# Kernel optimization log

Measured on AMD Instinct MI355X. Metric: run time of the kernel, lower is better.

Reference implementation:

```python
import jax, jax.numpy as jnp
import numpy as np
import math

N_HEAD = 16

def setup_inputs() -> dict:
    key = jax.random.key(0)
    k1, k2, k3, k4, k5 = jax.random.split(key, 5)
    B, T, C = 8, 1024, 1024
    scale = 0.02
    return {
        "x": jax.random.normal(k1, (B, T, C), dtype=jnp.float32),
        "w_attn": jax.random.normal(k2, (C, 3 * C), dtype=jnp.float32) * scale,
        "b_attn": jax.random.normal(k3, (3 * C,), dtype=jnp.float32) * scale,
        "w_proj": jax.random.normal(k4, (C, C), dtype=jnp.float32) * scale,
        "b_proj": jax.random.normal(k5, (C,), dtype=jnp.float32) * scale,
    }

def reference(x, w_attn, b_attn, w_proj, b_proj):
    B, T, C = x.shape
    H = N_HEAD
    hd = C // H
    # QKV projection: [B,T,3C]
    qkv = jnp.einsum("btc,cd->btd", x, w_attn) + b_attn
    q, k, v = jnp.split(qkv, 3, axis=-1)
    # [B,T,C] -> [B,H,T,hd]
    def heads(t):
        return t.reshape(B, T, H, hd).transpose(0, 2, 1, 3)
    q, k, v = heads(q), heads(k), heads(v)
    # scaled QK^T: [B,H,T,T]
    att = jnp.einsum("bhqd,bhkd->bhqk", q, k) * (1.0 / math.sqrt(hd))
    # causal mask (tril of block_size cropped to T)
    causal = jnp.tril(jnp.ones((T, T), dtype=bool))
    att = jnp.where(causal, att, jnp.float32(-jnp.inf))
    att = jax.nn.softmax(att, axis=-1)
    # attention-weighted values: [B,H,T,hd] -> [B,T,C]
    y = jnp.einsum("bhqk,bhkd->bhqd", att, v)
    y = y.transpose(0, 2, 1, 3).reshape(B, T, C)
    # output projection
    return jnp.einsum("btc,cd->btd", y, w_proj) + b_proj
```

## Files before the change

### kernel.cpp

```cpp
#include <hip/hip_runtime.h>

typedef __bf16 bf16x8 __attribute__((ext_vector_type(8)));
typedef float f32x4 __attribute__((ext_vector_type(4)));
typedef unsigned short u16;
typedef unsigned int u32;
typedef unsigned long long u64;

__device__ __forceinline__ u16 f2bf(float f) {
  u32 u = __builtin_bit_cast(u32, f);
  u32 r = (u + 0x7FFFu + ((u >> 16) & 1u)) >> 16;
  return (u16)r;
}

__device__ __forceinline__ void gload_lds16(const u16* g, u16* l) {
  __builtin_amdgcn_global_load_lds(
      (const __attribute__((address_space(1))) u32*)g,
      (__attribute__((address_space(3))) u32*)l, 16, 0, 0);
}

__global__ void cast_x_kernel(const float* __restrict__ in, u16* __restrict__ out, int n4) {
  int i = blockIdx.x * blockDim.x + threadIdx.x;
  if (i >= n4) return;
  float4 v = ((const float4*)in)[i];
  uint2 o;
  o.x = (u32)f2bf(v.x) | ((u32)f2bf(v.y) << 16);
  o.y = (u32)f2bf(v.z) | ((u32)f2bf(v.w) << 16);
  ((uint2*)out)[i] = o;
}

__global__ void transpose_cast_kernel(const float* __restrict__ in, u16* __restrict__ out,
                                      int K, int N) {
  __shared__ float tile[32][33];
  int n0 = blockIdx.x * 32, k0 = blockIdx.y * 32;
  int tx = threadIdx.x & 31, ty = threadIdx.x >> 5;
#pragma unroll
  for (int i = 0; i < 32; i += 8)
    tile[ty + i][tx] = in[(size_t)(k0 + ty + i) * N + n0 + tx];
  __syncthreads();
#pragma unroll
  for (int i = 0; i < 32; i += 8)
    out[(size_t)(n0 + ty + i) * K + k0 + tx] = f2bf(tile[tx][ty + i]);
}

template <int MODE>
__global__ __launch_bounds__(256, 3) void gemm_bf16(
    const u16* __restrict__ A, const u16* __restrict__ Bt,
    const float* __restrict__ bias, u16* __restrict__ out_q,
    float* __restrict__ out_f, int M, int N, int K) {
  __shared__ alignas(16) u16 As[128 * 64];
  __shared__ alignas(16) u16 Bs[128 * 64];
  const int tiles_n = N >> 7;
  const int bid0 = blockIdx.x;
  const int cpx = (int)gridDim.x >> 3;
  const int swz = (bid0 & 7) * cpx + (bid0 >> 3);
  const int tm = swz / tiles_n;
  const int tn = swz % tiles_n;
  const int tid = threadIdx.x;
  const int wave = tid >> 6, lane = tid & 63;
  const int wr = (wave >> 1) * 64, wc = (wave & 1) * 64;
  const int lr = lane & 15, lg = lane >> 4;

  f32x4 acc[4][4] = {};
  const size_t a_base = (size_t)(tm * 128) * K;
  const size_t b_base = (size_t)(tn * 128) * K;

  for (int k0 = 0; k0 < K; k0 += 64) {
#pragma unroll
    for (int i = 0; i < 4; ++i) {
      int c = i * 256 + tid;
      int row = c >> 3, ch = c & 7;
      int sw = (ch ^ (row & 7)) * 8;
      gload_lds16(A + a_base + (size_t)row * K + k0 + sw, &As[c * 8]);
      gload_lds16(Bt + b_base + (size_t)row * K + k0 + sw, &Bs[c * 8]);
    }
    __syncthreads();
    bf16x8 af[4][2], bfr[4][2];
#pragma unroll
    for (int m = 0; m < 4; ++m) {
      int row = wr + m * 16 + lr;
#pragma unroll
      for (int kk = 0; kk < 2; ++kk)
        af[m][kk] = *(const bf16x8*)&As[(row * 64 + kk * 32 + lg * 8) ^ ((row & 7) << 3)];
    }
#pragma unroll
    for (int n = 0; n < 4; ++n) {
      int row = wc + n * 16 + lr;
#pragma unroll
      for (int kk = 0; kk < 2; ++kk)
        bfr[n][kk] = *(const bf16x8*)&Bs[(row * 64 + kk * 32 + lg * 8) ^ ((row & 7) << 3)];
    }
#pragma unroll
    for (int m = 0; m < 4; ++m)
#pragma unroll
      for (int n = 0; n < 4; ++n) {
        if constexpr (MODE == 0) {
          acc[m][n] = __builtin_amdgcn_mfma_f32_16x16x32_bf16(bfr[n][0], af[m][0], acc[m][n], 0, 0, 0);
          acc[m][n] = __builtin_amdgcn_mfma_f32_16x16x32_bf16(bfr[n][1], af[m][1], acc[m][n], 0, 0, 0);
        } else {
          acc[m][n] = __builtin_amdgcn_mfma_f32_16x16x32_bf16(af[m][0], bfr[n][0], acc[m][n], 0, 0, 0);
          acc[m][n] = __builtin_amdgcn_mfma_f32_16x16x32_bf16(af[m][1], bfr[n][1], acc[m][n], 0, 0, 0);
        }
      }
    __syncthreads();
  }

  if constexpr (MODE == 0) {
    const int tok0 = tm * 128 + wr;
    const int col0 = tn * 128 + wc;
#pragma unroll
    for (int n = 0; n < 4; ++n) {
      int ncol = col0 + n * 16 + lg * 4;
      float4 bv = *(const float4*)&bias[ncol];
      int which = ncol >> 10, c = ncol & 1023;
      int h = c >> 6, d = c & 63;
#pragma unroll
      for (int m = 0; m < 4; ++m) {
        int tok = tok0 + m * 16 + lr;
        int b = tok >> 10, t = tok & 1023;
        union { u16 s[4]; uint2 v; } pk;
        pk.s[0] = f2bf(acc[m][n][0] + bv.x);
        pk.s[1] = f2bf(acc[m][n][1] + bv.y);
        pk.s[2] = f2bf(acc[m][n][2] + bv.z);
        pk.s[3] = f2bf(acc[m][n][3] + bv.w);
        *(uint2*)&out_q[(size_t)which * 8388608 + ((((size_t)b * 16 + h) * 1024 + t) << 6) + d] = pk.v;
      }
    }
  } else if constexpr (MODE == 2) {
    const int tok0 = tm * 128 + wr;
    const int col0 = tn * 128 + wc;
#pragma unroll
    for (int n = 0; n < 4; ++n) {
      int ncol = col0 + n * 16 + lr;
      float bv = bias[ncol];
      int h = ncol >> 6, d = ncol & 63;
#pragma unroll
      for (int m = 0; m < 4; ++m) {
        int t0 = tok0 + m * 16 + lg * 4;
        int b = t0 >> 10, t = t0 & 1023;
        union { u16 s[4]; uint2 v; } pk;
        pk.s[0] = f2bf(acc[m][n][0] + bv);
        pk.s[1] = f2bf(acc[m][n][1] + bv);
        pk.s[2] = f2bf(acc[m][n][2] + bv);
        pk.s[3] = f2bf(acc[m][n][3] + bv);
        *(uint2*)&out_q[(((size_t)b * 16 + h) * 64 + d) * 1024 + t] = pk.v;
      }
    }
  } else {
    const int row0 = tm * 128 + wr;
    const int col0 = tn * 128 + wc;
#pragma unroll
    for (int n = 0; n < 4; ++n) {
      int col = col0 + n * 16 + lr;
      float bv = bias[col];
#pragma unroll
      for (int m = 0; m < 4; ++m)
#pragma unroll
        for (int r = 0; r < 4; ++r) {
          int mrow = row0 + m * 16 + lg * 4 + r;
          out_f[(size_t)mrow * N + col] = acc[m][n][r] + bv;
        }
    }
  }
}

__global__ __launch_bounds__(256, 2) void attn_kernel(
    const u16* __restrict__ Qb, const u16* __restrict__ Kb,
    const u16* __restrict__ Vb, u16* __restrict__ yb) {
  __shared__ alignas(16) u16 Ks[128 * 64];
  __shared__ alignas(16) u16 Vt[64 * 128];
  __shared__ alignas(16) u16 Pl[4][32 * 64];

  const int bid = blockIdx.x;
  const int xcd = bid & 7, j = bid >> 3;
  const int bh = ((j >> 2) << 3) + xcd;
  const int pr = j & 3;
  const size_t hb = (size_t)bh * 65536;
  const int tid = threadIdx.x, w = tid >> 6, lane = tid & 63;
  const int lr = lane & 15, lg = lane >> 4;
  const int b = bh >> 4, h = bh & 15;
  const float C2 = 0.18033688011112042f;

  for (int pass = 0; pass < 2; ++pass) {
    const int qt = pass ? (7 - pr) : pr;
    const int q0 = qt * 128 + w * 32;

    bf16x8 qf[2][2];
#pragma unroll
    for (int mi = 0; mi < 2; ++mi)
#pragma unroll
      for (int ks = 0; ks < 2; ++ks)
        qf[mi][ks] = *(const bf16x8*)&Qb[hb + (size_t)(q0 + mi * 16 + lr) * 64 + ks * 32 + lg * 8];

    float l_run[2] = {0.f, 0.f};
    f32x4 o[2][4] = {};

    const int nkt = qt + 1;
    for (int kt = 0; kt < nkt; ++kt) {
#pragma unroll
      for (int i = 0; i < 4; ++i) {
        int c = i * 256 + tid;
        int row = c >> 3, ch = c & 7;
        gload_lds16(Kb + hb + (size_t)(kt * 128 + row) * 64 + ((ch ^ (row & 7)) * 8), &Ks[c * 8]);
      }
#pragma unroll
      for (int i = 0; i < 4; ++i) {
        int c = i * 256 + tid;
        int row = c >> 4, ch = c & 15;
        gload_lds16(Vb + hb + (size_t)row * 1024 + kt * 128 + ((ch ^ (row & 15)) * 8), &Vt[c * 8]);
      }
      __syncthreads();

      f32x4 s[8][2] = {};
      __builtin_amdgcn_s_setprio(1);
#pragma unroll
      for (int ni = 0; ni < 8; ++ni) {
        int krow = ni * 16 + lr;
        bf16x8 kf0 = *(const bf16x8*)&Ks[(krow * 64 + lg * 8) ^ ((krow & 7) << 3)];
        bf16x8 kf1 = *(const bf16x8*)&Ks[(krow * 64 + 32 + lg * 8) ^ ((krow & 7) << 3)];
#pragma unroll
        for (int mi = 0; mi < 2; ++mi) {
          s[ni][mi] = __builtin_amdgcn_mfma_f32_16x16x32_bf16(kf0, qf[mi][0], s[ni][mi], 0, 0, 0);
          s[ni][mi] = __builtin_amdgcn_mfma_f32_16x16x32_bf16(kf1, qf[mi][1], s[ni][mi], 0, 0, 0);
        }
      }
      __builtin_amdgcn_s_setprio(0);

      const bool need_mask = (kt == qt);
#pragma unroll
      for (int mi = 0; mi < 2; ++mi) {
        if (need_mask) {
#pragma unroll
          for (int ni = 0; ni < 8; ++ni)
#pragma unroll
            for (int r = 0; r < 4; ++r) {
              int ka = kt * 128 + ni * 16 + lg * 4 + r;
              int qa = q0 + mi * 16 + lr;
              if (ka > qa) s[ni][mi][r] = -1e30f;
            }
        }
        float ps[8];
#pragma unroll
        for (int ni = 0; ni < 8; ++ni) {
#pragma unroll
          for (int r = 0; r < 4; ++r)
            s[ni][mi][r] = __builtin_amdgcn_exp2f(s[ni][mi][r] * C2);
          ps[ni] = (s[ni][mi][0] + s[ni][mi][1]) + (s[ni][mi][2] + s[ni][mi][3]);
        }
        l_run[mi] += ((ps[0] + ps[1]) + (ps[2] + ps[3])) + ((ps[4] + ps[5]) + (ps[6] + ps[7]));
      }
#pragma unroll
      for (int hh = 0; hh < 2; ++hh) {
#pragma unroll
        for (int mi = 0; mi < 2; ++mi) {
          int qrow = mi * 16 + lr;
          int sw = (qrow & 7) << 3;
#pragma unroll
          for (int nq = 0; nq < 4; ++nq) {
            int ni = hh * 4 + nq;
            u32 plo, phi;
            asm("v_cvt_pk_bf16_f32 %0, %1, %2" : "=v"(plo) : "v"(s[ni][mi][0]), "v"(s[ni][mi][1]));
            asm("v_cvt_pk_bf16_f32 %0, %1, %2" : "=v"(phi) : "v"(s[ni][mi][2]), "v"(s[ni][mi][3]));
            u64 pv = (u64)plo | ((u64)phi << 32);
            int e = (qrow * 64 + nq * 16 + lg * 4) ^ sw;
            *(u64*)&Pl[w][e] = pv;
          }
        }
        asm volatile("s_waitcnt lgkmcnt(0)" ::: "memory");
        __builtin_amdgcn_s_setprio(1);
#pragma unroll
        for (int kh = 0; kh < 2; ++kh) {
          int ksl = hh * 2 + kh;
          bf16x8 pf[2];
#pragma unroll
          for (int mi = 0; mi < 2; ++mi) {
            int prow = mi * 16 + lr;
            pf[mi] = *(const bf16x8*)&Pl[w][(prow * 64 + kh * 32 + lg * 8) ^ ((prow & 7) << 3)];
          }
#pragma unroll
          for (int nd = 0; nd < 4; ++nd) {
            int vrow = nd * 16 + lr;
            bf16x8 vf = *(const bf16x8*)&Vt[(vrow * 128 + ksl * 32 + lg * 8) ^ ((vrow & 15) << 3)];
#pragma unroll
            for (int mi = 0; mi < 2; ++mi)
              o[mi][nd] = __builtin_amdgcn_mfma_f32_16x16x32_bf16(pf[mi], vf, o[mi][nd], 0, 0, 0);
          }
        }
        __builtin_amdgcn_s_setprio(0);
      }
      __syncthreads();
    }

#pragma unroll
    for (int mi = 0; mi < 2; ++mi) {
      float lt = l_run[mi];
      lt += __shfl_xor(lt, 16);
      lt += __shfl_xor(lt, 32);
      f32x4 inv;
#pragma unroll
      for (int r = 0; r < 4; ++r) inv[r] = 1.f / __shfl(lt, lg * 4 + r);
#pragma unroll
      for (int nd = 0; nd < 4; ++nd)
#pragma unroll
        for (int r = 0; r < 4; ++r) {
          int t = q0 + mi * 16 + lg * 4 + r;
          int c = h * 64 + nd * 16 + lr;
          yb[((size_t)b * 1024 + t) * 1024 + c] = f2bf(o[mi][nd][r] * inv[r]);
        }
    }
    __syncthreads();
  }
}

extern "C" void kernel_launch(void* const* d_in, const int* in_sizes, int n_in,
                              void* d_out, int out_size, void* d_ws, size_t ws_size,
                              hipStream_t stream) {
  const float* x = (const float*)d_in[0];
  const float* w_attn = (const float*)d_in[1];
  const float* b_attn = (const float*)d_in[2];
  const float* w_proj = (const float*)d_in[3];
  const float* b_proj = (const float*)d_in[4];
  float* out = (float*)d_out;

  u16* ws = (u16*)d_ws;
  u16* xb = ws;
  u16* watT = xb + 8388608;
  u16* wpT = watT + 3145728;
  u16* Qb = wpT + 1048576;
  u16* Vt = Qb + 2 * 8388608;
  u16* yb = xb;

  cast_x_kernel<<<8192, 256, 0, stream>>>(x, xb, 2097152);
  {
    dim3 g(96, 32);
    transpose_cast_kernel<<<g, 256, 0, stream>>>(w_attn, watT, 1024, 3072);
  }
  {
    dim3 g(32, 32);
    transpose_cast_kernel<<<g, 256, 0, stream>>>(w_proj, wpT, 1024, 1024);
  }
  gemm_bf16<0><<<64 * 16, 256, 0, stream>>>(xb, watT, b_attn, Qb, nullptr, 8192, 2048, 1024);
  gemm_bf16<2><<<64 * 8, 256, 0, stream>>>(xb, watT + (size_t)2048 * 1024, b_attn + 2048, Vt,
                                           nullptr, 8192, 1024, 1024);
  attn_kernel<<<512, 256, 0, stream>>>(Qb, Qb + 8388608, Vt, yb);
  gemm_bf16<1><<<64 * 8, 256, 0, stream>>>(yb, wpT, b_proj, nullptr, out, 8192, 1024, 1024);
}
```

Baseline: 149.9 us.

## Add 256x256-tile pipelined QK projection GEMM with interleaved staging

Replaces the 128x128-tile QK projection GEMM with a new 512-thread kernel that computes 256x256 output tiles. It double-buffers LDS loads through global_load_lds, stages quarter tiles between the MFMA phases, and raises wave priority around the MFMA bursts. The goal is more reuse per byte loaded and hiding global-load latency behind compute. In exchange it needs 128KB of LDS per block and launches only 256 blocks, which lowers occupancy and may fill the CUs unevenly. The old MODE 0 path is removed from the template.

```diff
diff --git a/kernel.cpp b/kernel.cpp
--- a/kernel.cpp
+++ b/kernel.cpp
@@ -40,6 +40,153 @@
 #pragma unroll
   for (int i = 0; i < 32; i += 8)
     out[(size_t)(n0 + ty + i) * K + k0 + tx] = f2bf(tile[tx][ty + i]);
+}
+
+__global__ __launch_bounds__(512, 2) void gemm256qk(
+    const u16* __restrict__ A, const u16* __restrict__ Bt,
+    const float* __restrict__ bias, u16* __restrict__ out_q,
+    int M, int N, int K) {
+  __shared__ alignas(16) u16 lds[2][2][256 * 64];
+  const int tiles_n = N >> 8;
+  const int bid = blockIdx.x;
+  const int cpx = (int)gridDim.x >> 3;
+  const int swz = (bid & 7) * cpx + (bid >> 3);
+  const int tm = swz / tiles_n, tn = swz % tiles_n;
+  const int tid = threadIdx.x, lane = tid & 63;
+  const int w = tid >> 6, wm = w >> 2, wn = w & 3;
+  const int lr = lane & 15, lg = lane >> 4;
+  const int NT = K >> 6;
+
+  f32x4 acc[2][2][4][2] = {};
+
+  auto stage = [&](int t, int which) {
+    const int isB = which & 1, half = which >> 1;
+    const u16* mat = isB ? Bt : A;
+    const int row0 = (isB ? tn : tm) * 256 + half * 128;
+    u16* lbase = &lds[t & 1][isB][half * 8192];
+#pragma unroll
+    for (int j = 0; j < 2; ++j) {
+      int c = tid + j * 512;
+      int k8 = (c & 7) ^ ((c >> 3) & 7);
+      int row = c >> 3;
+      gload_lds16(mat + (size_t)(row0 + row) * K + t * 64 + k8 * 8, lbase + c * 8);
+    }
+  };
+  auto rdA = [&](int cur, int mh, int m, int kk) -> bf16x8 {
+    int row = mh * 128 + wm * 64 + m * 16 + lr;
+    int e = (row * 64 + kk * 32 + lg * 8) ^ ((row & 7) << 3);
+    return *(const bf16x8*)&lds[cur][0][e];
+  };
+  auto rdB = [&](int cur, int nh, int n, int kk) -> bf16x8 {
+    int row = nh * 128 + wn * 32 + n * 16 + lr;
+    int e = (row * 64 + kk * 32 + lg * 8) ^ ((row & 7) << 3);
+    return *(const bf16x8*)&lds[cur][1][e];
+  };
+
+  stage(0, 0); stage(0, 1); stage(0, 2); stage(0, 3);
+  stage(1, 0); stage(1, 1); stage(1, 2);
+  asm volatile("s_waitcnt vmcnt(6)" ::: "memory");
+  __builtin_amdgcn_s_barrier();
+
+  bf16x8 af[4][2], b0[2][2], b1[2][2];
+  for (int t = 0; t < NT; ++t) {
+    const int cur = t & 1;
+#pragma unroll
+    for (int m = 0; m < 4; ++m)
+#pragma unroll
+      for (int kk = 0; kk < 2; ++kk) af[m][kk] = rdA(cur, 0, m, kk);
+#pragma unroll
+    for (int n = 0; n < 2; ++n)
+#pragma unroll
+      for (int kk = 0; kk < 2; ++kk) b0[n][kk] = rdB(cur, 0, n, kk);
+    if (t + 1 < NT) stage(t + 1, 3);
+    __builtin_amdgcn_s_barrier();
+    asm volatile("s_waitcnt lgkmcnt(0)" ::: "memory");
+    __builtin_amdgcn_s_setprio(1);
+#pragma unroll
+    for (int m = 0; m < 4; ++m)
+#pragma unroll
+      for (int n = 0; n < 2; ++n)
+#pragma unroll
+        for (int kk = 0; kk < 2; ++kk)
+          acc[0][0][m][n] = __builtin_amdgcn_mfma_f32_16x16x32_bf16(b0[n][kk], af[m][kk], acc[0][0][m][n], 0, 0, 0);
+    __builtin_amdgcn_s_setprio(0);
+    __builtin_amdgcn_s_barrier();
+#pragma unroll
+    for (int n = 0; n < 2; ++n)
+#pragma unroll
+      for (int kk = 0; kk < 2; ++kk) b1[n][kk] = rdB(cur, 1, n, kk);
+    if (t + 2 < NT) stage(t + 2, 0);
+    __builtin_amdgcn_s_barrier();
+    asm volatile("s_waitcnt lgkmcnt(0)" ::: "memory");
+    __builtin_amdgcn_s_setprio(1);
+#pragma unroll
+    for (int m = 0; m < 4; ++m)
+#pragma unroll
+      for (int n = 0; n < 2; ++n)
+#pragma unroll
+        for (int kk = 0; kk < 2; ++kk)
+          acc[0][1][m][n] = __builtin_amdgcn_mfma_f32_16x16x32_bf16(b1[n][kk], af[m][kk], acc[0][1][m][n], 0, 0, 0);
+    __builtin_amdgcn_s_setprio(0);
+    __builtin_amdgcn_s_barrier();
+#pragma unroll
+    for (int m = 0; m < 4; ++m)
+#pragma unroll
+      for (int kk = 0; kk < 2; ++kk) af[m][kk] = rdA(cur, 1, m, kk);
+    if (t + 2 < NT) stage(t + 2, 1);
+    __builtin_amdgcn_s_barrier();
+    asm volatile("s_waitcnt lgkmcnt(0)" ::: "memory");
+    __builtin_amdgcn_s_setprio(1);
+#pragma unroll
+    for (int m = 0; m < 4; ++m)
+#pragma unroll
+      for (int n = 0; n < 2; ++n)
+#pragma unroll
+        for (int kk = 0; kk < 2; ++kk)
+          acc[1][0][m][n] = __builtin_amdgcn_mfma_f32_16x16x32_bf16(b0[n][kk], af[m][kk], acc[1][0][m][n], 0, 0, 0);
+    __builtin_amdgcn_s_setprio(0);
+    __builtin_amdgcn_s_barrier();
+    if (t + 2 < NT) stage(t + 2, 2);
+    __builtin_amdgcn_s_barrier();
+    __builtin_amdgcn_s_setprio(1);
+#pragma unroll
+    for (int m = 0; m < 4; ++m)
+#pragma unroll
+      for (int n = 0; n < 2; ++n)
+#pragma unroll
+        for (int kk = 0; kk < 2; ++kk)
+          acc[1][1][m][n] = __builtin_amdgcn_mfma_f32_16x16x32_bf16(b1[n][kk], af[m][kk], acc[1][1][m][n], 0, 0, 0);
+    __builtin_amdgcn_s_setprio(0);
+    if (t + 2 < NT) {
+      asm volatile("s_waitcnt vmcnt(6)" ::: "memory");
+    } else {
+      asm volatile("s_waitcnt vmcnt(0)" ::: "memory");
+    }
+    __builtin_amdgcn_s_barrier();
+  }
+
+#pragma unroll
+  for (int mh = 0; mh < 2; ++mh)
+#pragma unroll
+    for (int nh = 0; nh < 2; ++nh)
+#pragma unroll
+      for (int n = 0; n < 2; ++n) {
+        int ncol = tn * 256 + nh * 128 + wn * 32 + n * 16 + lg * 4;
+        float4 bv = *(const float4*)&bias[ncol];
+        int which = ncol >> 10, c = ncol & 1023;
+        int h = c >> 6, d = c & 63;
+#pragma unroll
+        for (int m = 0; m < 4; ++m) {
+          int tok = tm * 256 + mh * 128 + wm * 64 + m * 16 + lr;
+          int b = tok >> 10, t = tok & 1023;
+          union { u16 s[4]; uint2 v; } pk;
+          pk.s[0] = f2bf(acc[mh][nh][m][n][0] + bv.x);
+          pk.s[1] = f2bf(acc[mh][nh][m][n][1] + bv.y);
+          pk.s[2] = f2bf(acc[mh][nh][m][n][2] + bv.z);
+          pk.s[3] = f2bf(acc[mh][nh][m][n][3] + bv.w);
+          *(uint2*)&out_q[(size_t)which * 8388608 + ((((size_t)b * 16 + h) * 1024 + t) << 6) + d] = pk.v;
+        }
+      }
 }
 
 template <int MODE>
@@ -93,39 +240,13 @@
     for (int m = 0; m < 4; ++m)
 #pragma unroll
       for (int n = 0; n < 4; ++n) {
-        if constexpr (MODE == 0) {
-          acc[m][n] = __builtin_amdgcn_mfma_f32_16x16x32_bf16(bfr[n][0], af[m][0], acc[m][n], 0, 0, 0);
-          acc[m][n] = __builtin_amdgcn_mfma_f32_16x16x32_bf16(bfr[n][1], af[m][1], acc[m][n], 0, 0, 0);
-        } else {
-          acc[m][n] = __builtin_amdgcn_mfma_f32_16x16x32_bf16(af[m][0], bfr[n][0], acc[m][n], 0, 0, 0);
-          acc[m][n] = __builtin_amdgcn_mfma_f32_16x16x32_bf16(af[m][1], bfr[n][1], acc[m][n], 0, 0, 0);
-        }
+        acc[m][n] = __builtin_amdgcn_mfma_f32_16x16x32_bf16(af[m][0], bfr[n][0], acc[m][n], 0, 0, 0);
+        acc[m][n] = __builtin_amdgcn_mfma_f32_16x16x32_bf16(af[m][1], bfr[n][1], acc[m][n], 0, 0, 0);
       }
     __syncthreads();
   }
 
-  if constexpr (MODE == 0) {
-    const int tok0 = tm * 128 + wr;
-    const int col0 = tn * 128 + wc;
-#pragma unroll
-    for (int n = 0; n < 4; ++n) {
-      int ncol = col0 + n * 16 + lg * 4;
-      float4 bv = *(const float4*)&bias[ncol];
-      int which = ncol >> 10, c = ncol & 1023;
-      int h = c >> 6, d = c & 63;
-#pragma unroll
-      for (int m = 0; m < 4; ++m) {
-        int tok = tok0 + m * 16 + lr;
-        int b = tok >> 10, t = tok & 1023;
-        union { u16 s[4]; uint2 v; } pk;
-        pk.s[0] = f2bf(acc[m][n][0] + bv.x);
-        pk.s[1] = f2bf(acc[m][n][1] + bv.y);
-        pk.s[2] = f2bf(acc[m][n][2] + bv.z);
-        pk.s[3] = f2bf(acc[m][n][3] + bv.w);
-        *(uint2*)&out_q[(size_t)which * 8388608 + ((((size_t)b * 16 + h) * 1024 + t) << 6) + d] = pk.v;
-      }
-    }
-  } else if constexpr (MODE == 2) {
+  if constexpr (MODE == 2) {
     const int tok0 = tm * 128 + wr;
     const int col0 = tn * 128 + wc;
 #pragma unroll
@@ -338,7 +459,7 @@
     dim3 g(32, 32);
     transpose_cast_kernel<<<g, 256, 0, stream>>>(w_proj, wpT, 1024, 1024);
   }
-  gemm_bf16<0><<<64 * 16, 256, 0, stream>>>(xb, watT, b_attn, Qb, nullptr, 8192, 2048, 1024);
+  gemm256qk<<<256, 512, 0, stream>>>(xb, watT, b_attn, Qb, 8192, 2048, 1024);
   gemm_bf16<2><<<64 * 8, 256, 0, stream>>>(xb, watT + (size_t)2048 * 1024, b_attn + 2048, Vt,
                                            nullptr, 8192, 1024, 1024);
   attn_kernel<<<512, 256, 0, stream>>>(Qb, Qb + 8388608, Vt, yb);
```

After: 138.8 us (median of 2 runs). -7.4%, faster.
